# Kernel optimization log

Measured on AMD Instinct MI355X. Metric: run time of the kernel, lower is better.

Reference implementation:

```python
import jax, jax.numpy as jnp
import numpy as np

VOCAB = 50000
EMB = 512
HID = 1024
B = 256
W = 26


def setup_inputs() -> dict:
    key = jax.random.key(0)
    k0, k1, k2, k3, k4, k5, k6 = jax.random.split(key, 7)
    s = 1.0 / np.sqrt(HID)
    return {
        "ques_vec": jax.random.randint(k0, (B, W), 0, VOCAB + 1, dtype=jnp.int32),
        "ques_len": jax.random.randint(k1, (B,), 1, W + 1, dtype=jnp.int32),
        # nn.Linear(vocab, emb, bias=False).weight -> [emb, vocab]
        "W_emb": jax.random.normal(k2, (EMB, VOCAB), dtype=jnp.float32) * 0.02,
        # PyTorch LSTM params, gate order (i, f, g, o)
        "W_ih": jax.random.uniform(k3, (4 * HID, EMB), jnp.float32, -s, s),
        "W_hh": jax.random.uniform(k4, (4 * HID, HID), jnp.float32, -s, s),
        "b_ih": jax.random.uniform(k5, (4 * HID,), jnp.float32, -s, s),
        "b_hh": jax.random.uniform(k6, (4 * HID,), jnp.float32, -s, s),
    }


def reference(ques_vec, ques_len, W_emb, W_ih, W_hh, b_ih, b_hh):
    # one_hot(vocab+1)[:, :, 1:] @ W_emb.T  ==  gather of W_emb columns;
    # token 0 (pad) maps to the zero embedding.
    tok = ques_vec  # [B, W]
    emb = jnp.where(
        (tok > 0)[..., None],
        W_emb.T[jnp.maximum(tok - 1, 0)],  # [B, W, EMB]
        jnp.zeros((), dtype=W_emb.dtype),
    )
    emb = jnp.tanh(emb)  # tanh(0)=0 for pads, matches torch

    bias = b_ih + b_hh

    def step(carry, xt):
        h, c = carry
        gates = xt @ W_ih.T + h @ W_hh.T + bias  # [B, 4H]
        i, f, g, o = jnp.split(gates, 4, axis=-1)
        c = jax.nn.sigmoid(f) * c + jax.nn.sigmoid(i) * jnp.tanh(g)
        h = jax.nn.sigmoid(o) * jnpp_tanh(c) if False else jax.nn.sigmoid(o) * jnp.tanh(c)
        return (h, c), None

    h0 = jnp.zeros((tok.shape[0], HID), dtype=W_emb.dtype)
    (h_n, _), _ = jax.lax.scan(step, (h0, h0), jnp.swapaxes(emb, 0, 1))
    return h_n  # [B, HID] == h_n.view(B, -1) for 1-layer unidirectional LSTM
```

## Files before the change

### kernel.cpp

```cpp
#include <hip/hip_runtime.h>
#include <hip/hip_bf16.h>

#define VOCAB 50000
#define EMBD  512
#define HID   1024
#define NB    256
#define SEQW  26
#define MTOT  (SEQW * NB)
#define NGATE (4 * HID)

#define TRB 6256
#define CVB 4096
#define INB 1024

typedef short short8 __attribute__((ext_vector_type(8)));
typedef _Float16 half8 __attribute__((ext_vector_type(8)));
typedef float f32x4  __attribute__((ext_vector_type(4)));
typedef float f32x2  __attribute__((ext_vector_type(2)));

__device__ __forceinline__ unsigned short f16bits(_Float16 h) {
    union { _Float16 h; unsigned short u; } cv; cv.h = h; return cv.u;
}

__device__ __forceinline__ void gload16(const void* g, void* l) {
    __builtin_amdgcn_global_load_lds(
        (const __attribute__((address_space(1))) void*)g,
        (__attribute__((address_space(3))) void*)l, 16, 0, 0);
}

__device__ __forceinline__ float fsig(float x) {
    return __builtin_amdgcn_rcpf(1.0f + __expf(-x));
}
__device__ __forceinline__ float ftanh(float x) {
    return 2.0f * __builtin_amdgcn_rcpf(1.0f + __expf(-2.0f * x)) - 1.0f;
}

__global__ void pre_kernel(const float* __restrict__ W,
                           unsigned short* __restrict__ WT,
                           const float* __restrict__ Wih,
                           const float* __restrict__ Whh,
                           const float* __restrict__ b_ih,
                           const float* __restrict__ b_hh,
                           unsigned short* __restrict__ ih,
                           unsigned short* __restrict__ hh,
                           float* __restrict__ bsum,
                           unsigned short* __restrict__ hBuf,
                           unsigned int* __restrict__ bar) {
    int bx = blockIdx.x;
    int tid = threadIdx.x;
    if (bx < TRB) {
        __shared__ _Float16 tile[64][72];
        int v0 = (bx % 782) * 64;
        int e0 = (bx / 782) * 64;
        int e_loc = tid >> 2, q = tid & 3;
        int vq = q * 16;
        if (v0 + vq < VOCAB) {
            const float* src = W + (size_t)(e0 + e_loc) * VOCAB + v0 + vq;
            #pragma unroll
            for (int j = 0; j < 4; ++j) {
                f32x4 x = *(const f32x4*)(src + 4 * j);
                #pragma unroll
                for (int i = 0; i < 4; ++i)
                    tile[vq + 4 * j + i][e_loc] = (_Float16)x[i];
            }
        }
        __syncthreads();
        int v_loc = tid >> 2;
        int ec = q * 16;
        int v = v0 + v_loc;
        if (v < VOCAB) {
            short8* dst = (short8*)(WT + (size_t)v * EMBD + e0 + ec);
            dst[0] = *(const short8*)&tile[v_loc][ec];
            dst[1] = *(const short8*)&tile[v_loc][ec + 8];
        }
    } else if (bx < TRB + CVB) {
        int j = bx - TRB;
        if (tid == 0) bsum[j] = b_ih[j] + b_hh[j];
        for (int col = tid; col < EMBD; col += blockDim.x)
            ih[(size_t)j * EMBD + col] = f16bits((_Float16)Wih[(size_t)j * EMBD + col]);
        for (int col = tid; col < HID; col += blockDim.x)
            hh[(size_t)j * HID + col] = f16bits((_Float16)Whh[(size_t)j * HID + col]);
    } else {
        int idx = (bx - TRB - CVB) * 256 + tid;
        hBuf[idx] = 0;
        if (idx < 4096) bar[idx] = 0;
    }
}

__global__ void embed_kernel(const int* __restrict__ qv,
                             const unsigned short* __restrict__ WT,
                             unsigned short* __restrict__ eHi) {
    int pair = blockIdx.x * 4 + (threadIdx.x >> 6);
    int t = pair >> 8, b = pair & 255;
    int lane = threadIdx.x & 63;
    int tok = qv[b * SEQW + t];
    short8 out = {};
    if (tok > 0) {
        short8 v = *(const short8*)(WT + (size_t)(tok - 1) * EMBD + lane * 8);
        #pragma unroll
        for (int i = 0; i < 8; ++i) {
            union { short s; _Float16 h; } cv; cv.s = v[i];
            out[i] = (short)f16bits((_Float16)tanhf((float)cv.h));
        }
    }
    *(short8*)(eHi + (size_t)pair * EMBD + lane * 8) = out;
}

__global__ __launch_bounds__(512, 2) void pregemm_kernel(
    const unsigned short* __restrict__ eHi,
    const unsigned short* __restrict__ ih,
    const float* __restrict__ bsum,
    unsigned short* __restrict__ G0h)
{
    __shared__ char smem[65536];

    int id = blockIdx.x;
    int xcd = id & 7, lid = id >> 3;
    int pc = xcd * 4 + (lid & 3);
    int pm = lid >> 2;
    int m0 = pm * 128;

    int tid = threadIdx.x;
    int w = tid >> 6;
    int mh = w >> 2, nh = w & 3;
    int lane = tid & 63;
    int col16 = lane & 15, g4 = lane >> 4;

    int sr = lane >> 3, sc = lane & 7;
    int ra0 = w * 16 + sr, ra1 = ra0 + 8;
    const char* eB = (const char*)eHi;
    const char* iB = (const char*)ih;
    size_t aOffG0 = (size_t)(m0 + ra0) * 1024 + (size_t)(((sc ^ (ra0 & 7))) * 16);
    size_t aOffG1 = (size_t)(m0 + ra1) * 1024 + (size_t)(((sc ^ (ra1 & 7))) * 16);
    int gb0 = (ra0 >> 5) * 1024 + pc * 32 + (ra0 & 31);
    int gb1 = (ra1 >> 5) * 1024 + pc * 32 + (ra1 & 31);
    size_t bOffG0 = (size_t)gb0 * 1024 + (size_t)(((sc ^ (ra0 & 7))) * 16);
    size_t bOffG1 = (size_t)gb1 * 1024 + (size_t)(((sc ^ (ra1 & 7))) * 16);
    int ldsRow0 = (w * 16) * 128;
    int ldsRow1 = (w * 16 + 8) * 128;

    f32x4 acc[4][2];
    #pragma unroll
    for (int fm = 0; fm < 4; ++fm)
        #pragma unroll
        for (int fn = 0; fn < 2; ++fn)
            acc[fm][fn] = (f32x4){0.f, 0.f, 0.f, 0.f};

    int swb = col16 & 7;
    int aRow[4], bRow[2];
    #pragma unroll
    for (int fm = 0; fm < 4; ++fm) aRow[fm] = (mh * 64 + fm * 16 + col16) * 128;
    #pragma unroll
    for (int fn = 0; fn < 2; ++fn) bRow[fn] = (nh * 32 + fn * 16 + col16) * 128;

#define STAGE(kb, buf) do { \
        int kby = (kb) * 128; \
        char* aD = smem + (buf) * 16384; \
        char* bD = smem + 32768 + (buf) * 16384; \
        gload16(eB + aOffG0 + kby, aD + ldsRow0); \
        gload16(eB + aOffG1 + kby, aD + ldsRow1); \
        gload16(iB + bOffG0 + kby, bD + ldsRow0); \
        gload16(iB + bOffG1 + kby, bD + ldsRow1); \
    } while (0)

    STAGE(0, 0);
    #pragma unroll
    for (int kb = 0; kb < 8; ++kb) {
        int cur = kb & 1;
        __syncthreads();
        if (kb < 7) STAGE(kb + 1, cur ^ 1);
        const char* aS = smem + cur * 16384;
        const char* bS = smem + 32768 + cur * 16384;
        #pragma unroll
        for (int kk = 0; kk < 2; ++kk) {
            int co = ((kk * 4 + g4) ^ swb) * 16;
            half8 bF[2];
            #pragma unroll
            for (int fn = 0; fn < 2; ++fn)
                bF[fn] = *(const half8*)(const void*)(bS + bRow[fn] + co);
            #pragma unroll
            for (int fm = 0; fm < 4; ++fm) {
                half8 aF = *(const half8*)(const void*)(aS + aRow[fm] + co);
                #pragma unroll
                for (int fn = 0; fn < 2; ++fn)
                    acc[fm][fn] = __builtin_amdgcn_mfma_f32_16x16x32_f16(
                        aF, bF[fn], acc[fm][fn], 0, 0, 0);
            }
        }
    }
#undef STAGE

    #pragma unroll
    for (int fn = 0; fn < 2; ++fn) {
        int cp = nh * 32 + fn * 16 + col16;
        int gate = cp >> 5;
        int jh = pc * 32 + (cp & 31);
        int ct = jh >> 4, jl = jh & 15;
        int cidx = jl * 4 + gate;
        float bv = bsum[gate * HID + jh];
        #pragma unroll
        for (int fm = 0; fm < 4; ++fm)
            #pragma unroll
            for (int r = 0; r < 4; ++r) {
                int row = m0 + mh * 64 + fm * 16 + g4 * 4 + r;
                int t = row >> 8, b = row & 255;
                G0h[(((size_t)t * 64 + ct) * 256 + b) * 64 + cidx] =
                    f16bits((_Float16)(acc[fm][fn][r] + bv));
            }
    }
}

__global__ __launch_bounds__(512, 2) void lstm_persist(
    const unsigned short* __restrict__ hh,
    unsigned short* __restrict__ hBuf,
    const unsigned short* __restrict__ G0h,
    float* __restrict__ out,
    unsigned int* __restrict__ bar)
{
    extern __shared__ char smem[];
    float* gbuf = (float*)smem;

    int bx = blockIdx.x;
    int grp = bx & 7;
    int lid = bx >> 3;
    int m0  = grp * 32;
    int jh0 = lid * 32;

    int tid = threadIdx.x;
    int w = tid >> 6;
    int kq = w & 3, ch = w >> 2;
    int lane = tid & 63;
    int col16 = lane & 15, g4 = lane >> 4;

    unsigned int* flags = bar + grp * 32;

    half8 bB[4][8];
    #pragma unroll
    for (int nf = 0; nf < 4; ++nf) {
        int colp = ch * 64 + nf * 16 + col16;
        int gate = colp >> 5, c32 = colp & 31;
        const char* bRow = (const char*)hh +
            ((size_t)(gate * HID + jh0 + c32) * HID + kq * 256 + g4 * 8) * 2;
        #pragma unroll
        for (int kk = 0; kk < 8; ++kk)
            bB[nf][kk] = *(const half8*)(const void*)(bRow + kk * 64);
    }

    int swr = (col16 & 7) << 4;
    int ml = tid >> 4, sc16 = tid & 15, jl2 = sc16 * 2;
    int jh = jh0 + jl2;
    int ctE = jh >> 4, jlE = jh & 15;

    float cReg[2] = {0.f, 0.f};

    for (int t = 0; t < SEQW; ++t) {
        const unsigned short* hIn = hBuf + (size_t)t * NB * HID;
        unsigned short* hOut = hBuf + (size_t)(t + 1) * NB * HID;

        half8 g0;
        {
            const unsigned short* pg = G0h +
                (((size_t)t * 64 + ctE) * 256 + (m0 + ml)) * 64 + jlE * 4;
            g0 = *(const half8*)(const void*)pg;
        }

        f32x4 acc[2][4];
        #pragma unroll
        for (int mf = 0; mf < 2; ++mf)
            #pragma unroll
            for (int nf = 0; nf < 4; ++nf)
                acc[mf][nf] = (f32x4){0.f, 0.f, 0.f, 0.f};

        if (t > 0) {
            #pragma unroll
            for (int j = 0; j < 8; ++j) {
                int row = w * 4 + (j >> 1);
                int half_ = j & 1;
                int cs = (half_ * 64 + lane) ^ (row & 7);
                gload16((const char*)hIn + (size_t)(m0 + row) * 2048 + cs * 16,
                        smem + row * 2048 + half_ * 1024);
            }
            __syncthreads();

            #pragma unroll
            for (int kk = 0; kk < 8; ++kk) {
                int kb = kq * 512 + kk * 64 + g4 * 16;
                int kbs = kb ^ swr;
                half8 a0 = *(const half8*)(const void*)(smem + col16 * 2048 + kbs);
                half8 a1 = *(const half8*)(const void*)(smem + (col16 + 16) * 2048 + kbs);
                #pragma unroll
                for (int nf = 0; nf < 4; ++nf) {
                    acc[0][nf] = __builtin_amdgcn_mfma_f32_16x16x32_f16(a0, bB[nf][kk], acc[0][nf], 0, 0, 0);
                    acc[1][nf] = __builtin_amdgcn_mfma_f32_16x16x32_f16(a1, bB[nf][kk], acc[1][nf], 0, 0, 0);
                }
            }
        }
        __syncthreads();

        #pragma unroll
        for (int mf = 0; mf < 2; ++mf)
            #pragma unroll
            for (int nf = 0; nf < 4; ++nf) {
                int colp = ch * 64 + nf * 16 + col16;
                #pragma unroll
                for (int r = 0; r < 4; ++r)
                    gbuf[(kq * 32 + mf * 16 + g4 * 4 + r) * 132 + colp] = acc[mf][nf][r];
            }
        __syncthreads();

        float gv[4][2];
        #pragma unroll
        for (int g = 0; g < 4; ++g) {
            f32x2 s = {0.f, 0.f};
            #pragma unroll
            for (int q = 0; q < 4; ++q)
                s += *(const f32x2*)&gbuf[(q * 32 + ml) * 132 + g * 32 + jl2];
            gv[g][0] = s[0] + (float)g0[g];
            gv[g][1] = s[1] + (float)g0[4 + g];
        }

        float hN[2];
        #pragma unroll
        for (int u = 0; u < 2; ++u) {
            float si = fsig(gv[0][u]);
            float sf = fsig(gv[1][u]);
            float tg = ftanh(gv[2][u]);
            float so = fsig(gv[3][u]);
            float cN = sf * cReg[u] + si * tg;
            hN[u] = so * ftanh(cN);
            cReg[u] = cN;
        }
        size_t p = (size_t)(m0 + ml) * HID + jh;
        if (t == SEQW - 1) {
            *(f32x2*)(out + p) = (f32x2){hN[0], hN[1]};
        } else {
            unsigned int hv = (unsigned int)f16bits((_Float16)hN[0]) |
                              ((unsigned int)f16bits((_Float16)hN[1]) << 16);
            __hip_atomic_store((unsigned int*)(hOut + p), hv,
                               __ATOMIC_RELAXED, __HIP_MEMORY_SCOPE_AGENT);

            __syncthreads();
            unsigned int t1 = (unsigned int)(t + 1);
            if (tid == 0)
                __hip_atomic_store(flags + lid, t1,
                                   __ATOMIC_RELAXED, __HIP_MEMORY_SCOPE_AGENT);
            if (w == 0) {
                for (;;) {
                    unsigned int v = __hip_atomic_load(
                        flags + (lane & 31), __ATOMIC_RELAXED,
                        __HIP_MEMORY_SCOPE_AGENT);
                    if (__all(v >= t1)) break;
                    __builtin_amdgcn_s_sleep(1);
                }
            }
            __syncthreads();
        }
    }
}

extern "C" void kernel_launch(void* const* d_in, const int* in_sizes, int n_in,
                              void* d_out, int out_size, void* d_ws, size_t ws_size,
                              hipStream_t stream) {
    const int*   qv   = (const int*)d_in[0];
    const float* Wemb = (const float*)d_in[2];
    const float* Wih  = (const float*)d_in[3];
    const float* Whh  = (const float*)d_in[4];
    const float* b_ih = (const float*)d_in[5];
    const float* b_hh = (const float*)d_in[6];
    float* out = (float*)d_out;

    char* ws = (char*)d_ws;
    size_t off = 0;
    unsigned short* eHi  = (unsigned short*)(ws + off); off += (size_t)MTOT * EMBD * 2;
    unsigned short* ih   = (unsigned short*)(ws + off); off += (size_t)NGATE * EMBD * 2;
    unsigned short* hh   = (unsigned short*)(ws + off); off += (size_t)NGATE * HID * 2;
    unsigned short* hBuf = (unsigned short*)(ws + off); off += (size_t)(SEQW + 1) * NB * HID * 2;
    float* bsum          = (float*)(ws + off);          off += (size_t)NGATE * 4;
    unsigned int* bar    = (unsigned int*)(ws + off);   off += 16384;
    off = (off + 255) & ~(size_t)255;
    unsigned short* G0h  = (unsigned short*)(ws + off); off += (size_t)MTOT * NGATE * 2;
    unsigned short* WembT = (unsigned short*)G0h;

    pre_kernel<<<TRB + CVB + INB, 256, 0, stream>>>(
        Wemb, WembT, Wih, Whh, b_ih, b_hh, ih, hh, bsum, hBuf, bar);
    embed_kernel<<<MTOT / 4, 256, 0, stream>>>(qv, WembT, eHi);
    pregemm_kernel<<<1664, 512, 0, stream>>>(eHi, ih, bsum, G0h);

    lstm_persist<<<256, 512, 67584, stream>>>(hh, hBuf, G0h, out, bar);
}
```

Measured before the change: 191.4 us.

## Split each block's batch rows into two phases with deferred flag signaling

Each persistent block now processes its 32 batch rows as two 16-row halves, each synchronising on its own flag group, so one half's recurrence can proceed while the other waits. The flag publish is deferred until after the next barrier, which replaces the end-of-step barrier plus spin with a single wait before use. This aims to cut the cost of the global cross-block barrier per step by pipelining two independent sub-batches. In exchange, each step issues more, smaller MFMA passes, writes h with 16-bit atomic stores, and has more __syncthreads per step.

```diff
diff --git a/kernel.cpp b/kernel.cpp
--- a/kernel.cpp
+++ b/kernel.cpp
@@ -15,6 +15,7 @@
 
 typedef short short8 __attribute__((ext_vector_type(8)));
 typedef _Float16 half8 __attribute__((ext_vector_type(8)));
+typedef _Float16 half4 __attribute__((ext_vector_type(4)));
 typedef float f32x4  __attribute__((ext_vector_type(4)));
 typedef float f32x2  __attribute__((ext_vector_type(2)));
 
@@ -218,12 +219,11 @@
     unsigned int* __restrict__ bar)
 {
     extern __shared__ char smem[];
-    float* gbuf = (float*)smem;
+    float* gbuf = (float*)(smem + 32768);
 
     int bx = blockIdx.x;
-    int grp = bx & 7;
+    int k   = bx & 7;
     int lid = bx >> 3;
-    int m0  = grp * 32;
     int jh0 = lid * 32;
 
     int tid = threadIdx.x;
@@ -232,7 +232,8 @@
     int lane = tid & 63;
     int col16 = lane & 15, g4 = lane >> 4;
 
-    unsigned int* flags = bar + grp * 32;
+    int m0p[2]  = { k * 32, k * 32 + 16 };
+    unsigned int* flg[2] = { bar + (2 * k) * 32, bar + (2 * k + 1) * 32 };
 
     half8 bB[4][8];
     #pragma unroll
@@ -247,113 +248,111 @@
     }
 
     int swr = (col16 & 7) << 4;
-    int ml = tid >> 4, sc16 = tid & 15, jl2 = sc16 * 2;
-    int jh = jh0 + jl2;
+    int ml = tid >> 5, jl = tid & 31;
+    int jh = jh0 + jl;
     int ctE = jh >> 4, jlE = jh & 15;
 
-    float cReg[2] = {0.f, 0.f};
+    float cR[2] = {0.f, 0.f};
+    unsigned int* pendPtr = 0;
+    unsigned int pendVal = 0;
 
     for (int t = 0; t < SEQW; ++t) {
         const unsigned short* hIn = hBuf + (size_t)t * NB * HID;
         unsigned short* hOut = hBuf + (size_t)(t + 1) * NB * HID;
 
-        half8 g0;
-        {
-            const unsigned short* pg = G0h +
-                (((size_t)t * 64 + ctE) * 256 + (m0 + ml)) * 64 + jlE * 4;
-            g0 = *(const half8*)(const void*)pg;
-        }
-
-        f32x4 acc[2][4];
-        #pragma unroll
-        for (int mf = 0; mf < 2; ++mf)
+        #pragma unroll
+        for (int ph = 0; ph < 2; ++ph) {
+            int m0 = m0p[ph];
+
+            half4 g0;
+            {
+                const unsigned short* pg = G0h +
+                    (((size_t)t * 64 + ctE) * 256 + (m0 + ml)) * 64 + jlE * 4;
+                g0 = *(const half4*)(const void*)pg;
+            }
+
+            if (t > 0 && w == 0) {
+                unsigned int tv = (unsigned int)t;
+                for (;;) {
+                    unsigned int v = __hip_atomic_load(
+                        flg[ph] + (lane & 31), __ATOMIC_RELAXED,
+                        __HIP_MEMORY_SCOPE_AGENT);
+                    if (__all(v >= tv)) break;
+                    __builtin_amdgcn_s_sleep(1);
+                }
+            }
+            __syncthreads();
+
+            if (pendPtr && tid == 0)
+                __hip_atomic_store(pendPtr, pendVal,
+                                   __ATOMIC_RELAXED, __HIP_MEMORY_SCOPE_AGENT);
+            pendPtr = 0;
+
+            f32x4 acc[4];
             #pragma unroll
             for (int nf = 0; nf < 4; ++nf)
-                acc[mf][nf] = (f32x4){0.f, 0.f, 0.f, 0.f};
-
-        if (t > 0) {
-            #pragma unroll
-            for (int j = 0; j < 8; ++j) {
-                int row = w * 4 + (j >> 1);
-                int half_ = j & 1;
-                int cs = (half_ * 64 + lane) ^ (row & 7);
-                gload16((const char*)hIn + (size_t)(m0 + row) * 2048 + cs * 16,
-                        smem + row * 2048 + half_ * 1024);
+                acc[nf] = (f32x4){0.f, 0.f, 0.f, 0.f};
+
+            if (t > 0) {
+                #pragma unroll
+                for (int j = 0; j < 4; ++j) {
+                    int row = w * 2 + (j >> 1);
+                    int half_ = j & 1;
+                    int cs = (half_ * 64 + lane) ^ (row & 7);
+                    gload16((const char*)hIn + (size_t)(m0 + row) * 2048 + cs * 16,
+                            smem + row * 2048 + half_ * 1024);
+                }
+                __syncthreads();
+
+                #pragma unroll
+                for (int kk = 0; kk < 8; ++kk) {
+                    int kb = kq * 512 + kk * 64 + g4 * 16;
+                    half8 a0 = *(const half8*)(const void*)(
+                        smem + col16 * 2048 + (kb ^ swr));
+                    #pragma unroll
+                    for (int nf = 0; nf < 4; ++nf)
+                        acc[nf] = __builtin_amdgcn_mfma_f32_16x16x32_f16(
+                            a0, bB[nf][kk], acc[nf], 0, 0, 0);
+                }
             }
             __syncthreads();
 
-            #pragma unroll
-            for (int kk = 0; kk < 8; ++kk) {
-                int kb = kq * 512 + kk * 64 + g4 * 16;
-                int kbs = kb ^ swr;
-                half8 a0 = *(const half8*)(const void*)(smem + col16 * 2048 + kbs);
-                half8 a1 = *(const half8*)(const void*)(smem + (col16 + 16) * 2048 + kbs);
-                #pragma unroll
-                for (int nf = 0; nf < 4; ++nf) {
-                    acc[0][nf] = __builtin_amdgcn_mfma_f32_16x16x32_f16(a0, bB[nf][kk], acc[0][nf], 0, 0, 0);
-                    acc[1][nf] = __builtin_amdgcn_mfma_f32_16x16x32_f16(a1, bB[nf][kk], acc[1][nf], 0, 0, 0);
-                }
-            }
-        }
-        __syncthreads();
-
-        #pragma unroll
-        for (int mf = 0; mf < 2; ++mf)
             #pragma unroll
             for (int nf = 0; nf < 4; ++nf) {
                 int colp = ch * 64 + nf * 16 + col16;
                 #pragma unroll
                 for (int r = 0; r < 4; ++r)
-                    gbuf[(kq * 32 + mf * 16 + g4 * 4 + r) * 132 + colp] = acc[mf][nf][r];
-            }
-        __syncthreads();
-
-        float gv[4][2];
-        #pragma unroll
-        for (int g = 0; g < 4; ++g) {
-            f32x2 s = {0.f, 0.f};
-            #pragma unroll
-            for (int q = 0; q < 4; ++q)
-                s += *(const f32x2*)&gbuf[(q * 32 + ml) * 132 + g * 32 + jl2];
-            gv[g][0] = s[0] + (float)g0[g];
-            gv[g][1] = s[1] + (float)g0[4 + g];
-        }
-
-        float hN[2];
-        #pragma unroll
-        for (int u = 0; u < 2; ++u) {
-            float si = fsig(gv[0][u]);
-            float sf = fsig(gv[1][u]);
-            float tg = ftanh(gv[2][u]);
-            float so = fsig(gv[3][u]);
-            float cN = sf * cReg[u] + si * tg;
-            hN[u] = so * ftanh(cN);
-            cReg[u] = cN;
-        }
-        size_t p = (size_t)(m0 + ml) * HID + jh;
-        if (t == SEQW - 1) {
-            *(f32x2*)(out + p) = (f32x2){hN[0], hN[1]};
-        } else {
-            unsigned int hv = (unsigned int)f16bits((_Float16)hN[0]) |
-                              ((unsigned int)f16bits((_Float16)hN[1]) << 16);
-            __hip_atomic_store((unsigned int*)(hOut + p), hv,
-                               __ATOMIC_RELAXED, __HIP_MEMORY_SCOPE_AGENT);
-
+                    gbuf[(kq * 16 + g4 * 4 + r) * 132 + colp] = acc[nf][r];
+            }
             __syncthreads();
-            unsigned int t1 = (unsigned int)(t + 1);
-            if (tid == 0)
-                __hip_atomic_store(flags + lid, t1,
+
+            float gv[4];
+            #pragma unroll
+            for (int g = 0; g < 4; ++g) {
+                float s = 0.f;
+                #pragma unroll
+                for (int q = 0; q < 4; ++q)
+                    s += gbuf[(q * 16 + ml) * 132 + g * 32 + jl];
+                gv[g] = s + (float)g0[g];
+            }
+            float si = fsig(gv[0]);
+            float sf = fsig(gv[1]);
+            float tg = ftanh(gv[2]);
+            float so = fsig(gv[3]);
+            float cN = sf * cR[ph] + si * tg;
+            float hN = so * ftanh(cN);
+            cR[ph] = cN;
+
+            size_t p = (size_t)(m0 + ml) * HID + jh;
+            if (t == SEQW - 1) {
+                out[p] = hN;
+            } else {
+                __hip_atomic_store((unsigned short*)(hOut + p),
+                                   f16bits((_Float16)hN),
                                    __ATOMIC_RELAXED, __HIP_MEMORY_SCOPE_AGENT);
-            if (w == 0) {
-                for (;;) {
-                    unsigned int v = __hip_atomic_load(
-                        flags + (lane & 31), __ATOMIC_RELAXED,
-                        __HIP_MEMORY_SCOPE_AGENT);
-                    if (__all(v >= t1)) break;
-                    __builtin_amdgcn_s_sleep(1);
-                }
-            }
-            __syncthreads();
+                pendPtr = flg[ph] + lid;
+                pendVal = (unsigned int)(t + 1);
+            }
         }
     }
 }
@@ -386,5 +385,5 @@
     embed_kernel<<<MTOT / 4, 256, 0, stream>>>(qv, WembT, eHi);
     pregemm_kernel<<<1664, 512, 0, stream>>>(eHi, ih, bsum, G0h);
 
-    lstm_persist<<<256, 512, 67584, stream>>>(hh, hBuf, G0h, out, bar);
-}
+    lstm_persist<<<256, 512, 66560, stream>>>(hh, hBuf, G0h, out, bar);
+}
```

Result: no change. 192.0 us (+0.4%).

## Fuse embedding gather and tanh into transpose and pregemm A-loads

Applied to the files above, without the earlier changes.

Tanh is now applied once per vocabulary entry in the transpose stage, and the embed kernel is dropped. The pregemm kernel gathers embedding rows straight from the transposed table through token indices, with a zero row standing in for pads. This removes one launch and the intermediate embedding buffer write and read. In the persistent LSTM kernel the gate buffer moves to a separate shared-memory region so one barrier can be removed, which doubles dynamic LDS and may reduce occupancy. Tanh now runs on all 25.6M table entries instead of only the gathered ones.

```diff
diff --git a/kernel.cpp b/kernel.cpp
--- a/kernel.cpp
+++ b/kernel.cpp
@@ -45,7 +45,8 @@
                            unsigned short* __restrict__ hh,
                            float* __restrict__ bsum,
                            unsigned short* __restrict__ hBuf,
-                           unsigned int* __restrict__ bar) {
+                           unsigned int* __restrict__ bar,
+                           unsigned short* __restrict__ zrow) {
     int bx = blockIdx.x;
     int tid = threadIdx.x;
     if (bx < TRB) {
@@ -61,7 +62,7 @@
                 f32x4 x = *(const f32x4*)(src + 4 * j);
                 #pragma unroll
                 for (int i = 0; i < 4; ++i)
-                    tile[vq + 4 * j + i][e_loc] = (_Float16)x[i];
+                    tile[vq + 4 * j + i][e_loc] = (_Float16)ftanh(x[i]);
             }
         }
         __syncthreads();
@@ -84,30 +85,14 @@
         int idx = (bx - TRB - CVB) * 256 + tid;
         hBuf[idx] = 0;
         if (idx < 4096) bar[idx] = 0;
-    }
-}
-
-__global__ void embed_kernel(const int* __restrict__ qv,
-                             const unsigned short* __restrict__ WT,
-                             unsigned short* __restrict__ eHi) {
-    int pair = blockIdx.x * 4 + (threadIdx.x >> 6);
-    int t = pair >> 8, b = pair & 255;
-    int lane = threadIdx.x & 63;
-    int tok = qv[b * SEQW + t];
-    short8 out = {};
-    if (tok > 0) {
-        short8 v = *(const short8*)(WT + (size_t)(tok - 1) * EMBD + lane * 8);
-        #pragma unroll
-        for (int i = 0; i < 8; ++i) {
-            union { short s; _Float16 h; } cv; cv.s = v[i];
-            out[i] = (short)f16bits((_Float16)tanhf((float)cv.h));
-        }
-    }
-    *(short8*)(eHi + (size_t)pair * EMBD + lane * 8) = out;
+        if (idx < 512) zrow[idx] = 0;
+    }
 }
 
 __global__ __launch_bounds__(512, 2) void pregemm_kernel(
-    const unsigned short* __restrict__ eHi,
+    const int* __restrict__ qv,
+    const unsigned short* __restrict__ WT,
+    const unsigned short* __restrict__ zrow,
     const unsigned short* __restrict__ ih,
     const float* __restrict__ bsum,
     unsigned short* __restrict__ G0h)
@@ -128,10 +113,18 @@
 
     int sr = lane >> 3, sc = lane & 7;
     int ra0 = w * 16 + sr, ra1 = ra0 + 8;
-    const char* eB = (const char*)eHi;
+
+    int row0 = m0 + ra0, row1 = m0 + ra1;
+    int tok0 = qv[(row0 & 255) * SEQW + (row0 >> 8)];
+    int tok1 = qv[(row1 & 255) * SEQW + (row1 >> 8)];
+    const char* srcA0 = (tok0 > 0)
+        ? (const char*)WT + (size_t)(tok0 - 1) * 1024 + ((sc ^ (ra0 & 7)) * 16)
+        : (const char*)zrow + ((sc ^ (ra0 & 7)) * 16);
+    const char* srcA1 = (tok1 > 0)
+        ? (const char*)WT + (size_t)(tok1 - 1) * 1024 + ((sc ^ (ra1 & 7)) * 16)
+        : (const char*)zrow + ((sc ^ (ra1 & 7)) * 16);
+
     const char* iB = (const char*)ih;
-    size_t aOffG0 = (size_t)(m0 + ra0) * 1024 + (size_t)(((sc ^ (ra0 & 7))) * 16);
-    size_t aOffG1 = (size_t)(m0 + ra1) * 1024 + (size_t)(((sc ^ (ra1 & 7))) * 16);
     int gb0 = (ra0 >> 5) * 1024 + pc * 32 + (ra0 & 31);
     int gb1 = (ra1 >> 5) * 1024 + pc * 32 + (ra1 & 31);
     size_t bOffG0 = (size_t)gb0 * 1024 + (size_t)(((sc ^ (ra0 & 7))) * 16);
@@ -157,8 +150,8 @@
         int kby = (kb) * 128; \
         char* aD = smem + (buf) * 16384; \
         char* bD = smem + 32768 + (buf) * 16384; \
-        gload16(eB + aOffG0 + kby, aD + ldsRow0); \
-        gload16(eB + aOffG1 + kby, aD + ldsRow1); \
+        gload16(srcA0 + kby, aD + ldsRow0); \
+        gload16(srcA1 + kby, aD + ldsRow1); \
         gload16(iB + bOffG0 + kby, bD + ldsRow0); \
         gload16(iB + bOffG1 + kby, bD + ldsRow1); \
     } while (0)
@@ -218,7 +211,7 @@
     unsigned int* __restrict__ bar)
 {
     extern __shared__ char smem[];
-    float* gbuf = (float*)smem;
+    float* gbuf = (float*)(smem + 65536);
 
     int bx = blockIdx.x;
     int grp = bx & 7;
@@ -295,7 +288,6 @@
                 }
             }
         }
-        __syncthreads();
 
         #pragma unroll
         for (int mf = 0; mf < 2; ++mf)
@@ -371,20 +363,19 @@
 
     char* ws = (char*)d_ws;
     size_t off = 0;
-    unsigned short* eHi  = (unsigned short*)(ws + off); off += (size_t)MTOT * EMBD * 2;
+    unsigned short* WT   = (unsigned short*)(ws + off); off += (size_t)VOCAB * EMBD * 2;
     unsigned short* ih   = (unsigned short*)(ws + off); off += (size_t)NGATE * EMBD * 2;
     unsigned short* hh   = (unsigned short*)(ws + off); off += (size_t)NGATE * HID * 2;
     unsigned short* hBuf = (unsigned short*)(ws + off); off += (size_t)(SEQW + 1) * NB * HID * 2;
     float* bsum          = (float*)(ws + off);          off += (size_t)NGATE * 4;
     unsigned int* bar    = (unsigned int*)(ws + off);   off += 16384;
+    unsigned short* zrow = (unsigned short*)(ws + off); off += 1024;
     off = (off + 255) & ~(size_t)255;
     unsigned short* G0h  = (unsigned short*)(ws + off); off += (size_t)MTOT * NGATE * 2;
-    unsigned short* WembT = (unsigned short*)G0h;
 
     pre_kernel<<<TRB + CVB + INB, 256, 0, stream>>>(
-        Wemb, WembT, Wih, Whh, b_ih, b_hh, ih, hh, bsum, hBuf, bar);
-    embed_kernel<<<MTOT / 4, 256, 0, stream>>>(qv, WembT, eHi);
-    pregemm_kernel<<<1664, 512, 0, stream>>>(eHi, ih, bsum, G0h);
-
-    lstm_persist<<<256, 512, 67584, stream>>>(hh, hBuf, G0h, out, bar);
-}
+        Wemb, WT, Wih, Whh, b_ih, b_hh, ih, hh, bsum, hBuf, bar, zrow);
+    pregemm_kernel<<<1664, 512, 0, stream>>>(qv, WT, zrow, ih, bsum, G0h);
+
+    lstm_persist<<<256, 512, 133120, stream>>>(hh, hBuf, G0h, out, bar);
+}
```

Result: faster. 186.9 us (-2.3%).
